# Kernel optimization log

Hardware: AMD Instinct MI355X
Metric: run time of the kernel (lower is better)

Reference implementation:

```python
import jax, jax.numpy as jnp
import numpy as np

B, N, H, D = 1, 4096, 16, 64
C = H * D  # 1024
SCALE = D ** -0.5


def setup_inputs() -> dict:
    key = jax.random.key(0)
    k1, k2, k3, k4 = jax.random.split(key, 4)
    x = jax.random.normal(k1, (B, N, C), dtype=jnp.float32)
    # torch nn.Linear weights: [out_features, in_features]; y = x @ W.T + b
    w_qkv = jax.random.normal(k2, (3 * C, C), dtype=jnp.float32) * 0.02
    w_proj = jax.random.normal(k3, (C, C), dtype=jnp.float32) * 0.02
    b_proj = jax.random.normal(k4, (C,), dtype=jnp.float32) * 0.02
    return {"x": x, "w_qkv": w_qkv, "w_proj": w_proj, "b_proj": b_proj}


def reference(x, w_qkv, w_proj, b_proj):
    Bn, Nn, Cn = x.shape
    # fused QKV projection (no bias)
    qkv = jnp.einsum('bnc,oc->bno', x, w_qkv)            # [B,N,3C]
    qkv = qkv.reshape(Bn, Nn, 3, H, D)
    q = jnp.transpose(qkv[:, :, 0], (0, 2, 1, 3))        # [B,H,N,D]
    k = jnp.transpose(qkv[:, :, 1], (0, 2, 1, 3))
    v = jnp.transpose(qkv[:, :, 2], (0, 2, 1, 3))
    attn = jnp.einsum('bhnd,bhmd->bhnm', q, k) * SCALE   # [B,H,N,N]
    causal_mask = jnp.triu(jnp.ones((Nn, Nn), dtype=bool), k=1)
    attn = jnp.where(causal_mask, -jnp.inf, attn)
    attn = jax.nn.softmax(attn, axis=-1)
    out = jnp.einsum('bhnm,bhmd->bhnd', attn, v)          # [B,H,N,D]
    out = jnp.transpose(out, (0, 2, 1, 3)).reshape(Bn, Nn, Cn)
    out = jnp.einsum('bnc,oc->bno', out, w_proj) + b_proj
    return out
```

## Files before the change

kernel.cpp:

```cpp
#include <hip/hip_runtime.h>
#include <hip/hip_bf16.h>
#include <stdint.h>
#include <stddef.h>

using bf16 = __hip_bfloat16;
typedef short short8 __attribute__((ext_vector_type(8)));
typedef short short4v __attribute__((ext_vector_type(4)));
typedef short short2v __attribute__((ext_vector_type(2)));
typedef float f32x4 __attribute__((ext_vector_type(4)));

#define MFMA16(A, B, C) __builtin_amdgcn_mfma_f32_16x16x32_bf16(A, B, C, 0, 0, 0)
#define MFMA16K16(A, B, C) __builtin_amdgcn_mfma_f32_16x16x16bf16_1k(A, B, C, 0, 0, 0)
#define GLOAD_LDS(g, l) __builtin_amdgcn_global_load_lds( \
    (const __attribute__((address_space(1))) void*)(g),   \
    (__attribute__((address_space(3))) void*)(l), 16, 0, 0)

constexpr int AN  = 4096;
constexpr int NH  = 16;
constexpr int HD  = 64;
constexpr int CC  = 1024;
constexpr int C3  = 3072;
constexpr float QSCALE = 0.125f * 1.4426950408889634f;

__device__ inline short bf16s(float f) {
    return (short)((__float_as_uint(f) + 0x8000u) >> 16);
}
__device__ inline float bf2f(short s) {
    return __uint_as_float(((unsigned)(unsigned short)s) << 16);
}
__device__ inline bf16 sbf(short s) {
    union { short s; bf16 b; } u;
    u.s = s;
    return u.b;
}
#if __has_builtin(__builtin_amdgcn_cvt_pk_bf16_f32)
typedef __bf16 bf16x2 __attribute__((ext_vector_type(2)));
__device__ inline short2v pk2(float a, float b) {
    bf16x2 r = __builtin_amdgcn_cvt_pk_bf16_f32(a, b);
    return *(short2v*)&r;
}
#else
__device__ inline short2v pk2(float a, float b) {
    unsigned ua = __float_as_uint(a) + 0x8000u;
    unsigned ub = __float_as_uint(b) + 0x8000u;
    unsigned r  = __builtin_amdgcn_perm(ub, ua, 0x07060302);
    return *(short2v*)&r;
}
#endif
__device__ inline short4v pack4(float a, float b, float c, float d) {
    short2v lo = pk2(a, b), hi = pk2(c, d);
    short4v r;
    r[0] = lo[0]; r[1] = lo[1]; r[2] = hi[0]; r[3] = hi[1];
    return r;
}
#if __has_builtin(__builtin_amdgcn_exp2f)
#define FAST_EXP2(x) __builtin_amdgcn_exp2f(x)
#else
#define FAST_EXP2(x) exp2f(x)
#endif

__device__ inline int detect_mode_inline(const unsigned short* xraw, int lane) {
    int crazy = 0;
    #pragma unroll
    for (int i = 0; i < 4; ++i) {
        const unsigned short u = xraw[lane * 4 + i];
        const int e = (u >> 7) & 0xFF;
        if (e >= 134 || (e != 0 && e <= 110)) ++crazy;
    }
    #pragma unroll
    for (int off = 32; off > 0; off >>= 1)
        crazy += __shfl_down(crazy, off, 64);
    crazy = __shfl(crazy, 0, 64);
    return (crazy >= 8) ? 1 : 0;
}

__device__ inline void cast8(const void* __restrict__ src,
                             bf16* __restrict__ dst, int i, int m) {
    if (m) {
        const float* s = (const float*)src;
        float4 a = *(const float4*)(s + i);
        float4 b = *(const float4*)(s + i + 4);
        short8 o;
        short2v p0 = pk2(a.x, a.y), p1 = pk2(a.z, a.w);
        short2v p2 = pk2(b.x, b.y), p3 = pk2(b.z, b.w);
        o[0] = p0[0]; o[1] = p0[1]; o[2] = p1[0]; o[3] = p1[1];
        o[4] = p2[0]; o[5] = p2[1]; o[6] = p3[0]; o[7] = p3[1];
        *(short8*)(dst + i) = o;
    } else {
        *(short8*)(dst + i) = *(const short8*)((const short*)src + i);
    }
}

__global__ void cast_all(const void* __restrict__ x, const void* __restrict__ wq,
                         const void* __restrict__ wp, const void* __restrict__ bp,
                         bf16* __restrict__ xb, bf16* __restrict__ wqb,
                         bf16* __restrict__ wpb, float* __restrict__ biasf,
                         int* __restrict__ mode) {
    const int b = blockIdx.x;
    const int tid = threadIdx.x;
    const int m = detect_mode_inline((const unsigned short*)x, tid & 63);
    if (b < 2048) {
        cast8(x, xb, (b * 256 + tid) * 8, m);
    } else if (b < 3584) {
        cast8(wq, wqb, ((b - 2048) * 256 + tid) * 8, m);
    } else if (b < 4096) {
        cast8(wp, wpb, ((b - 3584) * 256 + tid) * 8, m);
    } else {
        #pragma unroll
        for (int i = tid; i < CC; i += 256)
            biasf[i] = m ? ((const float*)bp)[i] : bf2f(((const short*)bp)[i]);
        if (tid == 0) *mode = m;
    }
}

constexpr int BM = 128, BN = 128, BK = 32;

__global__ __launch_bounds__(256, 3) void gemm_qkv(
    const bf16* __restrict__ A, const bf16* __restrict__ Bw,
    bf16* __restrict__ Cout, bf16* __restrict__ vTout)
{
    __shared__ bf16 As[BM * BK];
    __shared__ bf16 Bs[BN * BK];

    const int tid  = threadIdx.x;
    const int wave = tid >> 6;
    const int lane = tid & 63;
    const int quad = lane >> 4;
    const int l16  = lane & 15;
    const int wr   = wave >> 1;
    const int wc   = wave & 1;
    const int m0   = blockIdx.y * BM;
    const int o0   = blockIdx.x * BN;

    const int srow = lane >> 2;
    const int scol = (lane & 3) * 8;

    f32x4 acc[4][4] = {};

    for (int k0 = 0; k0 < CC; k0 += BK) {
        __syncthreads();
        #pragma unroll
        for (int c = 0; c < 2; ++c) {
            const int rbase = wave * 32 + c * 16;
            GLOAD_LDS(A + (size_t)(m0 + rbase + srow) * CC + k0 + scol, &As[rbase * BK]);
            GLOAD_LDS(Bw + (size_t)(o0 + rbase + srow) * CC + k0 + scol, &Bs[rbase * BK]);
        }
        __syncthreads();

        short8 af[4], bfr[4];
        #pragma unroll
        for (int i = 0; i < 4; ++i)
            af[i] = *(const short8*)&As[(wr * 64 + i * 16 + l16) * BK + quad * 8];
        #pragma unroll
        for (int j = 0; j < 4; ++j)
            bfr[j] = *(const short8*)&Bs[(wc * 64 + j * 16 + l16) * BK + quad * 8];
        #pragma unroll
        for (int i = 0; i < 4; ++i)
            #pragma unroll
            for (int j = 0; j < 4; ++j)
                acc[i][j] = MFMA16(af[i], bfr[j], acc[i][j]);
    }

    if (o0 >= 2 * CC) {
        #pragma unroll
        for (int j = 0; j < 4; ++j) {
            const int vc = o0 - 2 * CC + wc * 64 + j * 16 + l16;
            #pragma unroll
            for (int i = 0; i < 4; ++i) {
                const int row0 = m0 + wr * 64 + i * 16 + quad * 4;
                *(short4v*)&vTout[(size_t)vc * AN + row0] =
                    pack4(acc[i][j][0], acc[i][j][1], acc[i][j][2], acc[i][j][3]);
            }
        }
        return;
    }
    const float qs = (o0 < CC) ? QSCALE : 1.0f;
    #pragma unroll
    for (int j = 0; j < 4; ++j) {
        const int col = o0 + wc * 64 + j * 16 + l16;
        #pragma unroll
        for (int i = 0; i < 4; ++i) {
            const int row = m0 + wr * 64 + i * 16 + quad * 4;
            #pragma unroll
            for (int r = 0; r < 2; ++r) {
                short2v p = pk2(acc[i][j][2 * r] * qs, acc[i][j][2 * r + 1] * qs);
                Cout[(size_t)(row + 2 * r) * C3 + col]     = sbf(p[0]);
                Cout[(size_t)(row + 2 * r + 1) * C3 + col] = sbf(p[1]);
            }
        }
    }
}

constexpr int PM = 128, PN = 64, PK = 32;

__global__ __launch_bounds__(256, 2) void gemm_proj(
    const bf16* __restrict__ A, const bf16* __restrict__ Bw,
    const float* __restrict__ bias, void* __restrict__ Cout,
    const int* __restrict__ mode)
{
    __shared__ bf16 As[PM * PK];
    __shared__ bf16 Bs[PN * PK];

    const int tid  = threadIdx.x;
    const int wave = tid >> 6;
    const int lane = tid & 63;
    const int quad = lane >> 4;
    const int l16  = lane & 15;
    const int wr   = wave >> 1;
    const int wc   = wave & 1;
    const int m0   = blockIdx.y * PM;
    const int o0   = blockIdx.x * PN;
    const bool f32out = (*mode != 0);

    const int srow = lane >> 2;
    const int scol = (lane & 3) * 8;

    f32x4 acc[4][2] = {};

    for (int k0 = 0; k0 < CC; k0 += PK) {
        __syncthreads();
        #pragma unroll
        for (int c = 0; c < 2; ++c) {
            const int rbase = wave * 32 + c * 16;
            GLOAD_LDS(A + (size_t)(m0 + rbase + srow) * CC + k0 + scol, &As[rbase * PK]);
        }
        {
            const int rbase = wave * 16;
            GLOAD_LDS(Bw + (size_t)(o0 + rbase + srow) * CC + k0 + scol, &Bs[rbase * PK]);
        }
        __syncthreads();

        short8 af[4], bfr[2];
        #pragma unroll
        for (int i = 0; i < 4; ++i)
            af[i] = *(const short8*)&As[(wr * 64 + i * 16 + l16) * PK + quad * 8];
        #pragma unroll
        for (int j = 0; j < 2; ++j)
            bfr[j] = *(const short8*)&Bs[(wc * 32 + j * 16 + l16) * PK + quad * 8];
        #pragma unroll
        for (int i = 0; i < 4; ++i)
            #pragma unroll
            for (int j = 0; j < 2; ++j)
                acc[i][j] = MFMA16(af[i], bfr[j], acc[i][j]);
    }

    #pragma unroll
    for (int j = 0; j < 2; ++j) {
        const int col = o0 + wc * 32 + j * 16 + l16;
        const float bv = bias[col];
        #pragma unroll
        for (int i = 0; i < 4; ++i) {
            const int row = m0 + wr * 64 + i * 16 + quad * 4;
            if (f32out) {
                #pragma unroll
                for (int r = 0; r < 4; ++r)
                    ((float*)Cout)[(size_t)(row + r) * CC + col] = acc[i][j][r] + bv;
            } else {
                #pragma unroll
                for (int r = 0; r < 2; ++r) {
                    short2v p = pk2(acc[i][j][2 * r] + bv, acc[i][j][2 * r + 1] + bv);
                    ((bf16*)Cout)[(size_t)(row + 2 * r) * CC + col]     = sbf(p[0]);
                    ((bf16*)Cout)[(size_t)(row + 2 * r + 1) * CC + col] = sbf(p[1]);
                }
            }
        }
    }
}

constexpr int TK = 64;

__global__ __launch_bounds__(256, 4) void attn5(
    const bf16* __restrict__ qkv, const bf16* __restrict__ vT,
    bf16* __restrict__ pOn, float* __restrict__ pl)
{
    __shared__ bf16 Ks[2][TK * HD];
    __shared__ bf16 Vs[2][HD * TK];

    const int tid  = threadIdx.x;
    const int wave = tid >> 6;
    const int lane = tid & 63;
    const int quad = lane >> 4;
    const int l16  = lane & 15;
    const int h7   = l16 & 7;
    const int h    = blockIdx.x & 15;
    const int t    = blockIdx.x >> 4;

    short4v ones;
    ones[0] = (short)0x3F80; ones[1] = (short)0x3F80;
    ones[2] = (short)0x3F80; ones[3] = (short)0x3F80;

    const int sr = lane >> 3;
    const int pc = lane & 7;

    #pragma unroll 1
    for (int pp = 0; pp < 2; ++pp) {
        const int tile = pp ? 63 - t : t;
        const int nIt  = tile + 1;
        const int i0   = pp ? ((64 - t) + 1) >> 1 : 0;
        const int i1   = pp ? 64 - t : (t + 2) >> 1;
        const int half = pp;
        const int qw   = tile * 64 + wave * 16;

        short8 qf0, qf1;
        {
            const bf16* qp = qkv + (size_t)(qw + l16) * C3 + h * HD + quad * 8;
            qf0 = *(const short8*)qp;
            qf1 = *(const short8*)(qp + 32);
        }

        f32x4 acc_l = {};
        f32x4 acc_o[4] = {};

        if (i0 < i1) {
            const bf16 *kp[2], *vp[2];
            #pragma unroll
            for (int c = 0; c < 2; ++c) {
                const int row = wave * 16 + c * 8 + sr;
                const int lc  = pc ^ (row & 7);
                kp[c] = qkv + (size_t)(i0 * TK + row) * C3 + CC + h * HD + lc * 8;
                vp[c] = vT + (size_t)(h * HD + row) * AN + i0 * TK + lc * 8;
            }
            auto stage = [&](int p) {
                #pragma unroll
                for (int c = 0; c < 2; ++c) {
                    const int rb = wave * 16 + c * 8;
                    GLOAD_LDS(kp[c], &Ks[p][rb * HD]);
                    GLOAD_LDS(vp[c], &Vs[p][rb * TK]);
                    kp[c] += (size_t)TK * C3;
                    vp[c] += TK;
                }
            };
            stage(0);
            __syncthreads();
            const bool hasdiag = (i1 == nIt);

            for (int it = i0; it < i1; ++it) {
                const int p = (it - i0) & 1;
                if (it + 1 < i1) stage(p ^ 1);

                f32x4 st[4];
                #pragma unroll
                for (int tt = 0; tt < 4; ++tt) {
                    const int row = tt * 16 + l16;
                    short8 kf0 = *(const short8*)&Ks[p][row * HD + ((quad ^ h7) * 8)];
                    short8 kf1 = *(const short8*)&Ks[p][row * HD + (((quad + 4) ^ h7) * 8)];
                    f32x4 a = {};
                    a = MFMA16(kf0, qf0, a);
                    a = MFMA16(kf1, qf1, a);
                    st[tt] = a;
                }

                if (hasdiag && it == i1 - 1) {
                    const int q = qw + l16;
                    const int kv0 = it * TK;
                    #pragma unroll
                    for (int tt = 0; tt < 4; ++tt)
                        #pragma unroll
                        for (int r = 0; r < 4; ++r) {
                            const int kv = kv0 + tt * 16 + quad * 4 + r;
                            st[tt][r] = (kv <= q) ? FAST_EXP2(st[tt][r]) : 0.0f;
                        }
                } else {
                    #pragma unroll
                    for (int tt = 0; tt < 4; ++tt)
                        #pragma unroll
                        for (int r = 0; r < 4; ++r)
                            st[tt][r] = FAST_EXP2(st[tt][r]);
                }

                #pragma unroll
                for (int tt = 0; tt < 4; ++tt) {
                    const short4v bp = pack4(st[tt][0], st[tt][1], st[tt][2], st[tt][3]);
                    acc_l = MFMA16K16(ones, bp, acc_l);
                    const int pc2 = (2 * tt + (quad >> 1)) ^ h7;
                    #pragma unroll
                    for (int dt = 0; dt < 4; ++dt) {
                        const int row = dt * 16 + l16;
                        short4v vf = *(const short4v*)&Vs[p][row * TK + pc2 * 8 + (quad & 1) * 4];
                        acc_o[dt] = MFMA16K16(vf, bp, acc_o[dt]);
                    }
                }
                __syncthreads();
            }
        }

        const size_t base = (size_t)half * AN * CC + (size_t)(qw + l16) * CC + h * HD;
        #pragma unroll
        for (int dt = 0; dt < 4; ++dt) {
            const int d0 = dt * 16 + quad * 4;
            *(short4v*)&pOn[base + d0] =
                pack4(acc_o[dt][0], acc_o[dt][1], acc_o[dt][2], acc_o[dt][3]);
        }
        if (quad == 0)
            pl[(size_t)half * NH * AN + (size_t)h * AN + qw + l16] = acc_l[0];
    }
}

__global__ __launch_bounds__(128) void combine_halves(
    const bf16* __restrict__ pOn, const float* __restrict__ pl,
    bf16* __restrict__ outp)
{
    const int q  = blockIdx.x;
    const int c0 = threadIdx.x * 8;
    const int h  = c0 >> 6;
    const float l0 = pl[(size_t)h * AN + q];
    const float l1 = pl[(size_t)NH * AN + (size_t)h * AN + q];
    const float L = l0 + l1;
    const float invL = (L > 0.f) ? 1.f / L : 0.f;
    const size_t off = (size_t)q * CC + c0;
    short8 o0 = *(const short8*)&pOn[off];
    short8 o1 = *(const short8*)&pOn[(size_t)AN * CC + off];
    short8 o;
    #pragma unroll
    for (int e = 0; e < 8; e += 2) {
        float v0 = (bf2f(o0[e])     + bf2f(o1[e]))     * invL;
        float v1 = (bf2f(o0[e + 1]) + bf2f(o1[e + 1])) * invL;
        short2v p = pk2(v0, v1);
        o[e] = p[0]; o[e + 1] = p[1];
    }
    *(short8*)&outp[off] = o;
}

extern "C" void kernel_launch(void* const* d_in, const int* in_sizes, int n_in,
                              void* d_out, int out_size, void* d_ws, size_t ws_size,
                              hipStream_t stream) {
    char* ws = (char*)d_ws;
    bf16*   qkv      = (bf16*)(ws);
    bf16*   attn_out = (bf16*)(ws + 25165824);
    bf16*   vT       = (bf16*)(ws + 33554432);
    bf16*   xb       = (bf16*)(ws + 41943040);
    bf16*   wqkvb    = (bf16*)(ws + 50331648);
    bf16*   wprojb   = (bf16*)(ws + 56623104);
    float*  biasf    = (float*)(ws + 58720256);
    int*    mode     = (int*)(ws + 58724352);
    bf16*   pOn      = (bf16*)(ws + 58728448);
    float*  pl       = (float*)(ws + 75505664);

    cast_all<<<dim3(4097), 256, 0, stream>>>(
        d_in[0], d_in[1], d_in[2], d_in[3], xb, wqkvb, wprojb, biasf, mode);

    gemm_qkv<<<dim3(C3 / BN, AN / BM), 256, 0, stream>>>(xb, wqkvb, qkv, vT);
    attn5<<<dim3(64 * NH), 256, 0, stream>>>(qkv, vT, pOn, pl);
    combine_halves<<<dim3(AN), 128, 0, stream>>>(pOn, pl, attn_out);
    gemm_proj<<<dim3(CC / PN, AN / PM), 256, 0, stream>>>(
        attn_out, wprojb, biasf, d_out, mode);
}
```

Measured before the change: 202.1 us.

## Rewrite attention with 32x32x16 MFMA, two waves per block and permlane swaps

The attention kernel moves from 16x16 MFMAs across four waves (16 queries each) to 32x32x16 bf16 MFMAs across two waves (32 queries each). The P fragment is rearranged from the QK^T accumulator layout into the PV operand layout in registers using v_permlane32_swap. The row-sum also goes through a 32x32 MFMA with a ones operand, and s_setprio is raised around the MFMA sections. The aim is fewer, larger MFMA instructions and more K/V reuse per LDS read, at the cost of more registers per wave, fewer waves per block, and changed launch bounds that may lower occupancy.

```diff
diff --git a/kernel.cpp b/kernel.cpp
--- a/kernel.cpp
+++ b/kernel.cpp
@@ -8,9 +8,11 @@
 typedef short short4v __attribute__((ext_vector_type(4)));
 typedef short short2v __attribute__((ext_vector_type(2)));
 typedef float f32x4 __attribute__((ext_vector_type(4)));
+typedef float f32x16 __attribute__((ext_vector_type(16)));
+typedef unsigned uintv4 __attribute__((ext_vector_type(4)));
 
 #define MFMA16(A, B, C) __builtin_amdgcn_mfma_f32_16x16x32_bf16(A, B, C, 0, 0, 0)
-#define MFMA16K16(A, B, C) __builtin_amdgcn_mfma_f32_16x16x16bf16_1k(A, B, C, 0, 0, 0)
+#define MFMA32(A, B, C) __builtin_amdgcn_mfma_f32_32x32x16_bf16(A, B, C, 0, 0, 0)
 #define GLOAD_LDS(g, l) __builtin_amdgcn_global_load_lds( \
     (const __attribute__((address_space(1))) void*)(g),   \
     (__attribute__((address_space(3))) void*)(l), 16, 0, 0)
@@ -47,11 +49,18 @@
     return *(short2v*)&r;
 }
 #endif
+__device__ inline unsigned pk2u(float a, float b) {
+    short2v p = pk2(a, b);
+    return *(unsigned*)&p;
+}
 __device__ inline short4v pack4(float a, float b, float c, float d) {
     short2v lo = pk2(a, b), hi = pk2(c, d);
     short4v r;
     r[0] = lo[0]; r[1] = lo[1]; r[2] = hi[0]; r[3] = hi[1];
     return r;
+}
+__device__ inline void plswap(unsigned &a, unsigned &b) {
+    asm("v_permlane32_swap_b32 %0, %1" : "+v"(a), "+v"(b));
 }
 #if __has_builtin(__builtin_amdgcn_exp2f)
 #define FAST_EXP2(x) __builtin_amdgcn_exp2f(x)
@@ -269,7 +278,7 @@
 
 constexpr int TK = 64;
 
-__global__ __launch_bounds__(256, 4) void attn5(
+__global__ __launch_bounds__(128, 2) void attn6(
     const bf16* __restrict__ qkv, const bf16* __restrict__ vT,
     bf16* __restrict__ pOn, float* __restrict__ pl)
 {
@@ -279,18 +288,19 @@
     const int tid  = threadIdx.x;
     const int wave = tid >> 6;
     const int lane = tid & 63;
-    const int quad = lane >> 4;
-    const int l16  = lane & 15;
-    const int h7   = l16 & 7;
+    const int l31  = lane & 31;
+    const int hh   = lane >> 5;
+    const int h7   = l31 & 7;
     const int h    = blockIdx.x & 15;
     const int t    = blockIdx.x >> 4;
 
-    short4v ones;
-    ones[0] = (short)0x3F80; ones[1] = (short)0x3F80;
-    ones[2] = (short)0x3F80; ones[3] = (short)0x3F80;
-
-    const int sr = lane >> 3;
-    const int pc = lane & 7;
+    short8 ones8;
+    #pragma unroll
+    for (int i = 0; i < 8; ++i) ones8[i] = (short)0x3F80;
+
+    const int sr  = lane >> 3;
+    const int pc  = lane & 7;
+    const int swz = pc ^ (sr & 7);
 
     #pragma unroll 1
     for (int pp = 0; pp < 2; ++pp) {
@@ -299,31 +309,32 @@
         const int i0   = pp ? ((64 - t) + 1) >> 1 : 0;
         const int i1   = pp ? 64 - t : (t + 2) >> 1;
         const int half = pp;
-        const int qw   = tile * 64 + wave * 16;
-
-        short8 qf0, qf1;
+        const int qw   = tile * 64 + wave * 32;
+        const int q    = qw + l31;
+
+        short8 qf[4];
         {
-            const bf16* qp = qkv + (size_t)(qw + l16) * C3 + h * HD + quad * 8;
-            qf0 = *(const short8*)qp;
-            qf1 = *(const short8*)(qp + 32);
-        }
-
-        f32x4 acc_l = {};
-        f32x4 acc_o[4] = {};
+            const bf16* qp = qkv + (size_t)q * C3 + h * HD + hh * 8;
+            #pragma unroll
+            for (int ki = 0; ki < 4; ++ki)
+                qf[ki] = *(const short8*)(qp + ki * 16);
+        }
+
+        f32x16 acc_l = {};
+        f32x16 acc_o[2] = {};
 
         if (i0 < i1) {
-            const bf16 *kp[2], *vp[2];
-            #pragma unroll
-            for (int c = 0; c < 2; ++c) {
-                const int row = wave * 16 + c * 8 + sr;
-                const int lc  = pc ^ (row & 7);
-                kp[c] = qkv + (size_t)(i0 * TK + row) * C3 + CC + h * HD + lc * 8;
-                vp[c] = vT + (size_t)(h * HD + row) * AN + i0 * TK + lc * 8;
+            const bf16 *kp[4], *vp[4];
+            #pragma unroll
+            for (int c = 0; c < 4; ++c) {
+                const int row = wave * 32 + c * 8 + sr;
+                kp[c] = qkv + (size_t)(i0 * TK + row) * C3 + CC + h * HD + swz * 8;
+                vp[c] = vT + (size_t)(h * HD + row) * AN + i0 * TK + swz * 8;
             }
             auto stage = [&](int p) {
                 #pragma unroll
-                for (int c = 0; c < 2; ++c) {
-                    const int rb = wave * 16 + c * 8;
+                for (int c = 0; c < 4; ++c) {
+                    const int rb = wave * 32 + c * 8;
                     GLOAD_LDS(kp[c], &Ks[p][rb * HD]);
                     GLOAD_LDS(vp[c], &Vs[p][rb * TK]);
                     kp[c] += (size_t)TK * C3;
@@ -338,61 +349,81 @@
                 const int p = (it - i0) & 1;
                 if (it + 1 < i1) stage(p ^ 1);
 
-                f32x4 st[4];
+                f32x16 st[2];
+                __builtin_amdgcn_s_setprio(1);
                 #pragma unroll
-                for (int tt = 0; tt < 4; ++tt) {
-                    const int row = tt * 16 + l16;
-                    short8 kf0 = *(const short8*)&Ks[p][row * HD + ((quad ^ h7) * 8)];
-                    short8 kf1 = *(const short8*)&Ks[p][row * HD + (((quad + 4) ^ h7) * 8)];
-                    f32x4 a = {};
-                    a = MFMA16(kf0, qf0, a);
-                    a = MFMA16(kf1, qf1, a);
-                    st[tt] = a;
+                for (int kt = 0; kt < 2; ++kt) {
+                    const int row = kt * 32 + l31;
+                    f32x16 a = {};
+                    #pragma unroll
+                    for (int ki = 0; ki < 4; ++ki) {
+                        short8 kf = *(const short8*)
+                            &Ks[p][row * HD + (((2 * ki + hh) ^ h7) * 8)];
+                        a = MFMA32(kf, qf[ki], a);
+                    }
+                    st[kt] = a;
                 }
+                __builtin_amdgcn_s_setprio(0);
 
                 if (hasdiag && it == i1 - 1) {
-                    const int q = qw + l16;
                     const int kv0 = it * TK;
                     #pragma unroll
-                    for (int tt = 0; tt < 4; ++tt)
+                    for (int kt = 0; kt < 2; ++kt)
                         #pragma unroll
-                        for (int r = 0; r < 4; ++r) {
-                            const int kv = kv0 + tt * 16 + quad * 4 + r;
-                            st[tt][r] = (kv <= q) ? FAST_EXP2(st[tt][r]) : 0.0f;
+                        for (int r = 0; r < 16; ++r) {
+                            const int kv = kv0 + kt * 32 + (r & 3) + 8 * (r >> 2) + 4 * hh;
+                            st[kt][r] = (kv <= q) ? FAST_EXP2(st[kt][r]) : 0.0f;
                         }
                 } else {
                     #pragma unroll
-                    for (int tt = 0; tt < 4; ++tt)
+                    for (int kt = 0; kt < 2; ++kt)
                         #pragma unroll
-                        for (int r = 0; r < 4; ++r)
-                            st[tt][r] = FAST_EXP2(st[tt][r]);
+                        for (int r = 0; r < 16; ++r)
+                            st[kt][r] = FAST_EXP2(st[kt][r]);
                 }
 
                 #pragma unroll
-                for (int tt = 0; tt < 4; ++tt) {
-                    const short4v bp = pack4(st[tt][0], st[tt][1], st[tt][2], st[tt][3]);
-                    acc_l = MFMA16K16(ones, bp, acc_l);
-                    const int pc2 = (2 * tt + (quad >> 1)) ^ h7;
+                for (int kt = 0; kt < 2; ++kt) {
                     #pragma unroll
-                    for (int dt = 0; dt < 4; ++dt) {
-                        const int row = dt * 16 + l16;
-                        short4v vf = *(const short4v*)&Vs[p][row * TK + pc2 * 8 + (quad & 1) * 4];
-                        acc_o[dt] = MFMA16K16(vf, bp, acc_o[dt]);
+                    for (int kc = 0; kc < 2; ++kc) {
+                        unsigned a0 = pk2u(st[kt][kc * 8 + 0], st[kt][kc * 8 + 1]);
+                        unsigned a1 = pk2u(st[kt][kc * 8 + 2], st[kt][kc * 8 + 3]);
+                        unsigned c0 = pk2u(st[kt][kc * 8 + 4], st[kt][kc * 8 + 5]);
+                        unsigned c1 = pk2u(st[kt][kc * 8 + 6], st[kt][kc * 8 + 7]);
+                        plswap(a0, c0);
+                        plswap(a1, c1);
+                        uintv4 fu;
+                        fu[0] = a0; fu[1] = a1; fu[2] = c0; fu[3] = c1;
+                        const short8 frag = *(const short8*)&fu;
+
+                        __builtin_amdgcn_s_setprio(1);
+                        acc_l = MFMA32(ones8, frag, acc_l);
+                        #pragma unroll
+                        for (int dt2 = 0; dt2 < 2; ++dt2) {
+                            const int row = dt2 * 32 + l31;
+                            short8 vf = *(const short8*)
+                                &Vs[p][row * TK + (((4 * kt + 2 * kc + hh) ^ h7) * 8)];
+                            acc_o[dt2] = MFMA32(vf, frag, acc_o[dt2]);
+                        }
+                        __builtin_amdgcn_s_setprio(0);
                     }
                 }
                 __syncthreads();
             }
         }
 
-        const size_t base = (size_t)half * AN * CC + (size_t)(qw + l16) * CC + h * HD;
-        #pragma unroll
-        for (int dt = 0; dt < 4; ++dt) {
-            const int d0 = dt * 16 + quad * 4;
-            *(short4v*)&pOn[base + d0] =
-                pack4(acc_o[dt][0], acc_o[dt][1], acc_o[dt][2], acc_o[dt][3]);
-        }
-        if (quad == 0)
-            pl[(size_t)half * NH * AN + (size_t)h * AN + qw + l16] = acc_l[0];
+        const size_t base = (size_t)half * AN * CC + (size_t)q * CC + h * HD;
+        #pragma unroll
+        for (int dt2 = 0; dt2 < 2; ++dt2)
+            #pragma unroll
+            for (int g = 0; g < 4; ++g) {
+                const int d0 = dt2 * 32 + g * 8 + 4 * hh;
+                *(short4v*)&pOn[base + d0] =
+                    pack4(acc_o[dt2][4 * g + 0], acc_o[dt2][4 * g + 1],
+                          acc_o[dt2][4 * g + 2], acc_o[dt2][4 * g + 3]);
+            }
+        if (hh == 0)
+            pl[(size_t)half * NH * AN + (size_t)h * AN + q] = acc_l[0];
     }
 }
 
@@ -440,7 +471,7 @@
         d_in[0], d_in[1], d_in[2], d_in[3], xb, wqkvb, wprojb, biasf, mode);
 
     gemm_qkv<<<dim3(C3 / BN, AN / BM), 256, 0, stream>>>(xb, wqkvb, qkv, vT);
-    attn5<<<dim3(64 * NH), 256, 0, stream>>>(qkv, vT, pOn, pl);
+    attn6<<<dim3(64 * NH), 128, 0, stream>>>(qkv, vT, pOn, pl);
     combine_halves<<<dim3(AN), 128, 0, stream>>>(pOn, pl, attn_out);
     gemm_proj<<<dim3(CC / PN, AN / PM), 256, 0, stream>>>(
         attn_out, wprojb, biasf, d_out, mode);
```

Result: faster. 193.5 us (-4.3%).
